# Kernel tuning notes

Measured on AMD Instinct MI355X. Metric: run time of the kernel, lower is better.

## Reference

```python
import jax, jax.numpy as jnp
import numpy as np

B, C, H, W = 8, 512, 64, 64
NUMS, V_C = 1024, 512
RATE = 0.999


def _normalize(x):
    # matches torch F.normalize(dim=-1, eps=1e-12)
    return x / jnp.clip(jnp.linalg.norm(x, axis=-1, keepdims=True), 1e-12)


def setup_inputs() -> dict:
    key = jax.random.key(0)
    k1, k2, k3 = jax.random.split(key, 3)
    return {
        "x": jax.random.normal(k1, (B, C, H, W), dtype=jnp.float32),
        "noise_feature": jax.random.normal(k2, (NUMS, C), dtype=jnp.float32),
        "std": jax.random.normal(k3, (NUMS, V_C), dtype=jnp.float32),
    }


def reference(x, noise_feature, std):
    b, c, h, w = x.shape
    # (b,c,h,w) -> (n,c)
    xf = jnp.transpose(x, (0, 2, 3, 1)).reshape(-1, c)
    m = jax.lax.stop_gradient(noise_feature)  # torch uses .data (no grad)
    xn = _normalize(xf)
    mn = _normalize(m)
    score = xn @ mn.T  # (n, k) cosine similarities

    # EMA codebook update (training path, update_flag=True)
    xd = jax.lax.stop_gradient(xf)
    embed_ind = jnp.argmax(score, axis=1)  # (n,)
    # segment_sum == x.T @ one_hot(ind), transposed; avoids dense one-hot GEMM
    embed_sum = jax.ops.segment_sum(xd, embed_ind, num_segments=NUMS)  # (k, c)
    counts = jax.ops.segment_sum(jnp.ones((xd.shape[0],), xd.dtype), embed_ind,
                                 num_segments=NUMS)  # (k,)
    embed_mean = embed_sum / (counts[:, None] + 1e-6)
    new_m = m * RATE + embed_mean * (1.0 - RATE)

    mn2 = _normalize(new_m)
    score2 = xn @ mn2.T  # (n, k)
    soft_label = jax.nn.softmax(score2, axis=1)
    out = (soft_label @ std).reshape(b, h, w, V_C)
    return out, score2
```

## Files before the change

### kernel.cpp

```cpp
#include <hip/hip_runtime.h>
#include <stdint.h>

#define NROWS 32768
#define CDIM  512
#define KCODES 1024
#define VC    512
#define LDP 72

typedef unsigned short u16;
typedef unsigned long long u64;
using bf16x8 = __attribute__((ext_vector_type(8))) __bf16;
using f32x4  = __attribute__((ext_vector_type(4))) float;

__device__ __forceinline__ float bf2f(u16 u){
  union { unsigned int i; float f; } x; x.i = ((unsigned int)u) << 16; return x.f;
}
__device__ __forceinline__ u16 f2bf(float f){
  union { float f; unsigned int i; } x; x.f = f;
  unsigned int u = x.i;
  u += 0x7fffu + ((u >> 16) & 1u);
  return (u16)(u >> 16);
}
__device__ __forceinline__ unsigned int pack2(u16 lo, u16 hi){
  return (unsigned int)lo | ((unsigned int)hi << 16);
}
__device__ __forceinline__ unsigned int fkey(float f){
  unsigned int u = __float_as_uint(f);
  return (u & 0x80000000u) ? ~u : (u | 0x80000000u);
}
__device__ __forceinline__ f32x4 mfma16(bf16x8 a, bf16x8 b, f32x4 c){
  return __builtin_amdgcn_mfma_f32_16x16x32_bf16(a, b, c, 0, 0, 0);
}
__device__ __forceinline__ void gload_lds16(const void* g, void* l){
  __builtin_amdgcn_global_load_lds(
      (const __attribute__((address_space(1))) unsigned int*)g,
      (__attribute__((address_space(3))) unsigned int*)l, 16, 0, 0);
}

__global__ __launch_bounds__(256) void k_transpose_x(const float* __restrict__ x,
                                                     u16* __restrict__ xf,
                                                     float* __restrict__ rsum){
  __shared__ float tile[64 * 64];
  int b  = blockIdx.z;
  int p0 = blockIdx.x * 64;
  int c0 = blockIdx.y * 64;
  int t  = threadIdx.x;
  const float* xb = x + (size_t)b * CDIM * 4096 + (size_t)c0 * 4096 + p0;

  int pl4 = (t & 15) * 4;
#pragma unroll
  for (int i = 0; i < 4; i++){
    int cl = i * 16 + (t >> 4);
    float4 v = *(const float4*)(xb + (size_t)cl * 4096 + pl4);
    *(float4*)(tile + cl * 64 + (pl4 ^ (cl & 0x38))) = v;
  }
  __syncthreads();

  int cl0 = (t & 7) * 8;
#pragma unroll
  for (int pass = 0; pass < 2; pass++){
    int pl = pass * 32 + (t >> 3);
    float v[8]; float s = 0.f;
#pragma unroll
    for (int j = 0; j < 8; j++){
      v[j] = tile[(cl0 + j) * 64 + (pl ^ cl0)];
      s += v[j] * v[j];
    }
    uint4 o;
    o.x = pack2(f2bf(v[0]), f2bf(v[1]));
    o.y = pack2(f2bf(v[2]), f2bf(v[3]));
    o.z = pack2(f2bf(v[4]), f2bf(v[5]));
    o.w = pack2(f2bf(v[6]), f2bf(v[7]));
    *(uint4*)(xf + (size_t)(b * 4096 + p0 + pl) * CDIM + c0 + cl0) = o;
    s += __shfl_xor(s, 1, 64);
    s += __shfl_xor(s, 2, 64);
    s += __shfl_xor(s, 4, 64);
    if ((t & 7) == 0) atomicAdd(rsum + b * 4096 + p0 + pl, s);
  }
}

__global__ __launch_bounds__(256) void k_rinv_fin(const float* __restrict__ rsum,
                                                  float* __restrict__ rinv){
  int i = blockIdx.x * 256 + threadIdx.x;
  rinv[i] = 1.0f / fmaxf(sqrtf(rsum[i]), 1e-12f);
}

__global__ __launch_bounds__(256) void k_norm_rows(const float* __restrict__ in,
                                                   u16* __restrict__ out){
  int row  = blockIdx.x * 4 + (threadIdx.x >> 6);
  int lane = threadIdx.x & 63;
  const float* r = in + (size_t)row * CDIM;
  float v[8]; float s = 0.f;
#pragma unroll
  for (int i = 0; i < 8; i++){ v[i] = r[lane + i * 64]; s += v[i] * v[i]; }
#pragma unroll
  for (int off = 32; off; off >>= 1) s += __shfl_xor(s, off, 64);
  float inv = 1.0f / fmaxf(sqrtf(s), 1e-12f);
#pragma unroll
  for (int i = 0; i < 8; i++) out[(size_t)row * CDIM + lane + i * 64] = f2bf(v[i] * inv);
}

__global__ __launch_bounds__(256) void k_transpose_std(const float* __restrict__ sd,
                                                       u16* __restrict__ stdT){
  __shared__ float tile[32][33];
  int k0 = blockIdx.x * 32;
  int v0 = blockIdx.y * 32;
  int tx = threadIdx.x, ty = threadIdx.y;
#pragma unroll
  for (int i = 0; i < 4; i++)
    tile[ty + i * 8][tx] = sd[(size_t)(k0 + ty + i * 8) * VC + v0 + tx];
  __syncthreads();
#pragma unroll
  for (int i = 0; i < 4; i++)
    stdT[(size_t)(v0 + ty + i * 8) * KCODES + k0 + tx] = f2bf(tile[tx][ty + i * 8]);
}

__global__ __launch_bounds__(256) void k_gemm1_am(const u16* __restrict__ xf,
                                                  const u16* __restrict__ mn,
                                                  u64* __restrict__ packed){
  __shared__ __align__(16) u16 As[128 * 64];
  __shared__ __align__(16) u16 Bs[128 * 64];
  int tid  = threadIdx.x;
  int wave = tid >> 6, lane = tid & 63;
  int wr = wave >> 1, wc = wave & 1;
  int quad = lane >> 4, l15 = lane & 15;
  int c0 = blockIdx.x * 128, r0 = blockIdx.y * 128;

  int srow = lane >> 3, schunk = lane & 7;
  const u16* ag = xf + (size_t)(r0 + wave * 8 + srow) * CDIM + schunk * 8;
  const u16* bg = mn + (size_t)(c0 + wave * 8 + srow) * CDIM + schunk * 8;
  u16* adst = As + wave * 8 * 64;
  u16* bdst = Bs + wave * 8 * 64;

  f32x4 acc[4][4];
#pragma unroll
  for (int rt = 0; rt < 4; rt++)
#pragma unroll
    for (int ct = 0; ct < 4; ct++) acc[rt][ct] = (f32x4)(0.f);

  for (int k0 = 0; k0 < CDIM; k0 += 64){
#pragma unroll
    for (int i = 0; i < 4; i++){
      gload_lds16(ag + (size_t)i * 32 * CDIM + k0, adst + i * 32 * 64);
      gload_lds16(bg + (size_t)i * 32 * CDIM + k0, bdst + i * 32 * 64);
    }
    __syncthreads();
#pragma unroll
    for (int ks = 0; ks < 2; ks++){
      bf16x8 af[4], bfr[4];
#pragma unroll
      for (int rt = 0; rt < 4; rt++)
        af[rt] = *(const bf16x8*)(As + (wr * 64 + rt * 16 + l15) * 64 + ks * 32 + quad * 8);
#pragma unroll
      for (int ct = 0; ct < 4; ct++)
        bfr[ct] = *(const bf16x8*)(Bs + (wc * 64 + ct * 16 + l15) * 64 + ks * 32 + quad * 8);
#pragma unroll
      for (int rt = 0; rt < 4; rt++)
#pragma unroll
        for (int ct = 0; ct < 4; ct++)
          acc[rt][ct] = mfma16(af[rt], bfr[ct], acc[rt][ct]);
    }
    __syncthreads();
  }

#pragma unroll
  for (int rt = 0; rt < 4; rt++){
#pragma unroll
    for (int q = 0; q < 4; q++){
      float bv = acc[rt][0][q];
      int   bc = c0 + wc * 64 + l15;
#pragma unroll
      for (int ct = 1; ct < 4; ct++){
        float v = acc[rt][ct][q];
        int   c = c0 + wc * 64 + ct * 16 + l15;
        if (v > bv){ bv = v; bc = c; }
      }
#pragma unroll
      for (int off = 1; off <= 8; off <<= 1){
        float ov = __shfl_xor(bv, off, 64);
        int   oc = __shfl_xor(bc, off, 64);
        if (ov > bv || (ov == bv && oc < bc)){ bv = ov; bc = oc; }
      }
      if (l15 == 0){
        int rg = r0 + wr * 64 + rt * 16 + quad * 4 + q;
        u64 key = ((u64)fkey(bv) << 32) | (unsigned int)(~(unsigned int)bc);
        atomicMax(packed + rg, key);
      }
    }
  }
}

__global__ __launch_bounds__(256) void k_gather(const u64* __restrict__ packed,
                                                const u16* __restrict__ xf,
                                                float* __restrict__ esum,
                                                float* __restrict__ counts){
  __shared__ float part[4][CDIM];
  __shared__ int   wcnt[4];
  int code = blockIdx.x;
  int tid = threadIdx.x, wave = tid >> 6, lane = tid & 63;
  float acc[8] = {0,0,0,0,0,0,0,0};
  int cnt = 0;
  for (int base = wave * 64; base < NROWS; base += 256){
    u64 pk = packed[base + lane];
    int cl = (int)(~(unsigned int)(pk & 0xffffffffull)) & (KCODES - 1);
    int match = (cl == code);
    u64 mask = __ballot(match);
    cnt += (int)__popcll(mask);
    while (mask){
      int b = __ffsll((long long)mask) - 1;
      mask &= mask - 1;
      int rr = base + b;
      uint4 v = *(const uint4*)(xf + (size_t)rr * CDIM + lane * 8);
      unsigned int w[4] = {v.x, v.y, v.z, v.w};
#pragma unroll
      for (int i = 0; i < 4; i++){
        acc[2 * i]     += bf2f((u16)(w[i] & 0xffffu));
        acc[2 * i + 1] += bf2f((u16)(w[i] >> 16));
      }
    }
  }
#pragma unroll
  for (int j = 0; j < 8; j++) part[wave][lane * 8 + j] = acc[j];
  if (lane == 0) wcnt[wave] = cnt;
  __syncthreads();
  for (int c = tid; c < CDIM; c += 256)
    esum[(size_t)code * CDIM + c] = part[0][c] + part[1][c] + part[2][c] + part[3][c];
  if (tid == 0) counts[code] = (float)(wcnt[0] + wcnt[1] + wcnt[2] + wcnt[3]);
}

__global__ __launch_bounds__(256) void k_newm(const float* __restrict__ m,
                                              const float* __restrict__ esum,
                                              const float* __restrict__ counts,
                                              u16* __restrict__ mn2){
  int row  = blockIdx.x * 4 + (threadIdx.x >> 6);
  int lane = threadIdx.x & 63;
  float cnt = counts[row];
  float sc  = 0.001f / (cnt + 1e-6f);
  float v[8]; float s = 0.f;
#pragma unroll
  for (int i = 0; i < 8; i++){
    int c = lane + i * 64;
    v[i] = m[(size_t)row * CDIM + c] * 0.999f + esum[(size_t)row * CDIM + c] * sc;
    s += v[i] * v[i];
  }
#pragma unroll
  for (int off = 32; off; off >>= 1) s += __shfl_xor(s, off, 64);
  float inv = 1.0f / fmaxf(sqrtf(s), 1e-12f);
#pragma unroll
  for (int i = 0; i < 8; i++) mn2[(size_t)row * CDIM + lane + i * 64] = f2bf(v[i] * inv);
}

__global__ __launch_bounds__(256) void k_gemm2(const u16* __restrict__ xf,
                                               const u16* __restrict__ mn2,
                                               const float* __restrict__ rinv,
                                               float* __restrict__ score2,
                                               float* __restrict__ pmax,
                                               float* __restrict__ psum){
  __shared__ __align__(16) u16 As[128 * 64];
  __shared__ __align__(16) u16 Bs[128 * 64];
  int tid  = threadIdx.x;
  int wave = tid >> 6, lane = tid & 63;
  int wr = wave >> 1, wc = wave & 1;
  int quad = lane >> 4, l15 = lane & 15;
  int c0 = blockIdx.x * 128, r0 = blockIdx.y * 128;

  int srow = lane >> 3, schunk = lane & 7;
  const u16* ag = xf  + (size_t)(r0 + wave * 8 + srow) * CDIM + schunk * 8;
  const u16* bg = mn2 + (size_t)(c0 + wave * 8 + srow) * CDIM + schunk * 8;
  u16* adst = As + wave * 8 * 64;
  u16* bdst = Bs + wave * 8 * 64;

  f32x4 acc[4][4];
#pragma unroll
  for (int rt = 0; rt < 4; rt++)
#pragma unroll
    for (int ct = 0; ct < 4; ct++) acc[rt][ct] = (f32x4)(0.f);

  for (int k0 = 0; k0 < CDIM; k0 += 64){
#pragma unroll
    for (int i = 0; i < 4; i++){
      gload_lds16(ag + (size_t)i * 32 * CDIM + k0, adst + i * 32 * 64);
      gload_lds16(bg + (size_t)i * 32 * CDIM + k0, bdst + i * 32 * 64);
    }
    __syncthreads();
#pragma unroll
    for (int ks = 0; ks < 2; ks++){
      bf16x8 af[4], bfr[4];
#pragma unroll
      for (int rt = 0; rt < 4; rt++)
        af[rt] = *(const bf16x8*)(As + (wr * 64 + rt * 16 + l15) * 64 + ks * 32 + quad * 8);
#pragma unroll
      for (int ct = 0; ct < 4; ct++)
        bfr[ct] = *(const bf16x8*)(Bs + (wc * 64 + ct * 16 + l15) * 64 + ks * 32 + quad * 8);
#pragma unroll
      for (int rt = 0; rt < 4; rt++)
#pragma unroll
        for (int ct = 0; ct < 4; ct++)
          acc[rt][ct] = mfma16(af[rt], bfr[ct], acc[rt][ct]);
    }
    __syncthreads();
  }

#pragma unroll
  for (int rt = 0; rt < 4; rt++){
#pragma unroll
    for (int q = 0; q < 4; q++){
      int grow = r0 + wr * 64 + rt * 16 + quad * 4 + q;
      float rv = rinv[grow];
      float v0 = acc[rt][0][q] * rv;
      float v1 = acc[rt][1][q] * rv;
      float v2 = acc[rt][2][q] * rv;
      float v3 = acc[rt][3][q] * rv;
      float* so = score2 + (size_t)grow * KCODES + c0 + wc * 64 + l15;
      so[0]  = v0;
      so[16] = v1;
      so[32] = v2;
      so[48] = v3;
      float mx = fmaxf(fmaxf(v0, v1), fmaxf(v2, v3));
#pragma unroll
      for (int off = 1; off <= 8; off <<= 1) mx = fmaxf(mx, __shfl_xor(mx, off, 64));
      float s = __expf(v0 - mx) + __expf(v1 - mx) + __expf(v2 - mx) + __expf(v3 - mx);
#pragma unroll
      for (int off = 1; off <= 8; off <<= 1) s += __shfl_xor(s, off, 64);
      if (l15 == 0){
        int pi = grow * 16 + blockIdx.x * 2 + wc;
        pmax[pi] = mx;
        psum[pi] = s;
      }
    }
  }
}

__global__ __launch_bounds__(256) void k_softcomb(const float* __restrict__ pmax,
                                                  const float* __restrict__ psum,
                                                  float* __restrict__ rowmax,
                                                  float* __restrict__ rsinv){
  int row = blockIdx.x * 256 + threadIdx.x;
  const float* pm = pmax + (size_t)row * 16;
  const float* ps = psum + (size_t)row * 16;
  float M = pm[0];
#pragma unroll
  for (int i = 1; i < 16; i++) M = fmaxf(M, pm[i]);
  float S = 0.f;
#pragma unroll
  for (int i = 0; i < 16; i++) S += ps[i] * __expf(pm[i] - M);
  rowmax[row] = M;
  rsinv[row]  = 1.0f / S;
}

__global__ __launch_bounds__(512) void k_gemm3(const float* __restrict__ score2,
                                               const float* __restrict__ rowmax,
                                               const float* __restrict__ rsinv,
                                               const u16* __restrict__ stdT,
                                               float* __restrict__ out){
  __shared__ __align__(16) u16 As[128 * LDP];
  __shared__ __align__(16) u16 Bs[256 * 64];
  int tid  = threadIdx.x;
  int wave = tid >> 6, lane = tid & 63;
  int wr = wave >> 2, wcol = wave & 3;
  int quad = lane >> 4, l15 = lane & 15;
  int c0 = blockIdx.x * 256, r0 = blockIdx.y * 128;
  int arow = tid >> 2, aq = tid & 3;

  int srow = lane >> 3, schunk = lane & 7;
  const u16* bg = stdT + (size_t)(c0 + wave * 8 + srow) * KCODES + schunk * 8;
  u16* bdst = Bs + wave * 8 * 64;

  float rmax = rowmax[r0 + arow];
  float rs   = rsinv [r0 + arow];

  f32x4 acc[4][4];
#pragma unroll
  for (int rt = 0; rt < 4; rt++)
#pragma unroll
    for (int ct = 0; ct < 4; ct++) acc[rt][ct] = (f32x4)(0.f);

  const float* ag = score2 + (size_t)(r0 + arow) * KCODES + aq * 16;

  for (int k0 = 0; k0 < KCODES; k0 += 64){
#pragma unroll
    for (int i = 0; i < 4; i++)
      gload_lds16(bg + (size_t)i * 64 * KCODES + k0, bdst + i * 64 * 64);
#pragma unroll
    for (int j = 0; j < 2; j++){
      float4 a = *(const float4*)(ag + k0 + j * 8);
      float4 b = *(const float4*)(ag + k0 + j * 8 + 4);
      uint4 o;
      o.x = pack2(f2bf(__expf(a.x - rmax) * rs), f2bf(__expf(a.y - rmax) * rs));
      o.y = pack2(f2bf(__expf(a.z - rmax) * rs), f2bf(__expf(a.w - rmax) * rs));
      o.z = pack2(f2bf(__expf(b.x - rmax) * rs), f2bf(__expf(b.y - rmax) * rs));
      o.w = pack2(f2bf(__expf(b.z - rmax) * rs), f2bf(__expf(b.w - rmax) * rs));
      *(uint4*)(As + arow * LDP + aq * 16 + j * 8) = o;
    }
    __syncthreads();
#pragma unroll
    for (int ks = 0; ks < 2; ks++){
      bf16x8 af[4], bfr[4];
#pragma unroll
      for (int rt = 0; rt < 4; rt++)
        af[rt] = *(const bf16x8*)(As + (wr * 64 + rt * 16 + l15) * LDP + ks * 32 + quad * 8);
#pragma unroll
      for (int ct = 0; ct < 4; ct++)
        bfr[ct] = *(const bf16x8*)(Bs + (wcol * 64 + ct * 16 + l15) * 64 + ks * 32 + quad * 8);
#pragma unroll
      for (int rt = 0; rt < 4; rt++)
#pragma unroll
        for (int ct = 0; ct < 4; ct++)
          acc[rt][ct] = mfma16(af[rt], bfr[ct], acc[rt][ct]);
    }
    __syncthreads();
  }
#pragma unroll
  for (int rt = 0; rt < 4; rt++){
#pragma unroll
    for (int q = 0; q < 4; q++){
      int grow = r0 + wr * 64 + rt * 16 + quad * 4 + q;
#pragma unroll
      for (int ct = 0; ct < 4; ct++){
        int gcol = c0 + wcol * 64 + ct * 16 + l15;
        out[(size_t)grow * VC + gcol] = acc[rt][ct][q];
      }
    }
  }
}

extern "C" void kernel_launch(void* const* d_in, const int* in_sizes, int n_in,
                              void* d_out, int out_size, void* d_ws, size_t ws_size,
                              hipStream_t stream){
  (void)in_sizes; (void)n_in; (void)out_size; (void)ws_size;
  const float* x      = (const float*)d_in[0];
  const float* m      = (const float*)d_in[1];
  const float* stdmat = (const float*)d_in[2];
  float* out    = (float*)d_out;
  float* score2 = out + (size_t)NROWS * VC;

  char* ws = (char*)d_ws;
  u16*   xf     = (u16*)  (ws + 0);
  u16*   mn     = (u16*)  (ws + 33554432);
  u16*   mn2    = (u16*)  (ws + 34603008);
  u16*   stdT   = (u16*)  (ws + 35651584);
  float* rinv   = (float*)(ws + 36700160);
  u64*   packed = (u64*)  (ws + 36831232);
  float* esum   = (float*)(ws + 37224448);
  float* counts = (float*)(ws + 39321600);
  float* rowmax = (float*)(ws + 39325696);
  float* rsinv  = (float*)(ws + 39456768);
  float* pmax   = (float*)(ws + 39587840);
  float* psum   = (float*)(ws + 41684992);
  float* rsum   = rowmax;

  hipMemsetAsync(packed, 0, (size_t)NROWS * 8, stream);
  hipMemsetAsync(rsum,   0, (size_t)NROWS * 4, stream);

  k_transpose_x  <<<dim3(64, 8, 8), 256, 0, stream>>>(x, xf, rsum);
  k_rinv_fin     <<<NROWS / 256, 256, 0, stream>>>(rsum, rinv);
  k_norm_rows    <<<KCODES / 4, 256, 0, stream>>>(m, mn);
  k_transpose_std<<<dim3(32, 16), dim3(32, 8), 0, stream>>>(stdmat, stdT);
  k_gemm1_am     <<<dim3(KCODES / 128, NROWS / 128), 256, 0, stream>>>(xf, mn, packed);
  k_gather       <<<KCODES, 256, 0, stream>>>(packed, xf, esum, counts);
  k_newm         <<<KCODES / 4, 256, 0, stream>>>(m, esum, counts, mn2);
  k_gemm2        <<<dim3(KCODES / 128, NROWS / 128), 256, 0, stream>>>(xf, mn2, rinv, score2, pmax, psum);
  k_softcomb     <<<NROWS / 256, 256, 0, stream>>>(pmax, psum, rowmax, rsinv);
  k_gemm3        <<<dim3(VC / 256, NROWS / 128), 512, 0, stream>>>(score2, rowmax, rsinv, stdT, out);
}
```

Measured before the change: 503.0 us.

## Widen softmax-GEMM tile to full output width and fuse small prep kernels

The final GEMM now gives each 512-thread block all 512 output columns. The fp32 score2 tile is read and exponentiated once per row instead of once per column half, which halves the traffic on the large score matrix and the softmax recomputation. The codebook-normalize and std-transpose kernels are merged into one launch. The row inverse-norm kernel is removed and its value is computed inline in the gemm2 epilogue from rsum. The trade-off is more accumulator registers and about 82KB of LDS per block, which lowers occupancy and leaves only one block per CU across a 256-block grid.

After: 514.1 us. 2.2% more time.

```diff
diff --git a/kernel.cpp b/kernel.cpp
--- a/kernel.cpp
+++ b/kernel.cpp
@@ -79,40 +79,37 @@
   }
 }
 
-__global__ __launch_bounds__(256) void k_rinv_fin(const float* __restrict__ rsum,
-                                                  float* __restrict__ rinv){
-  int i = blockIdx.x * 256 + threadIdx.x;
-  rinv[i] = 1.0f / fmaxf(sqrtf(rsum[i]), 1e-12f);
-}
-
-__global__ __launch_bounds__(256) void k_norm_rows(const float* __restrict__ in,
-                                                   u16* __restrict__ out){
-  int row  = blockIdx.x * 4 + (threadIdx.x >> 6);
-  int lane = threadIdx.x & 63;
-  const float* r = in + (size_t)row * CDIM;
-  float v[8]; float s = 0.f;
-#pragma unroll
-  for (int i = 0; i < 8; i++){ v[i] = r[lane + i * 64]; s += v[i] * v[i]; }
-#pragma unroll
-  for (int off = 32; off; off >>= 1) s += __shfl_xor(s, off, 64);
-  float inv = 1.0f / fmaxf(sqrtf(s), 1e-12f);
-#pragma unroll
-  for (int i = 0; i < 8; i++) out[(size_t)row * CDIM + lane + i * 64] = f2bf(v[i] * inv);
-}
-
-__global__ __launch_bounds__(256) void k_transpose_std(const float* __restrict__ sd,
-                                                       u16* __restrict__ stdT){
-  __shared__ float tile[32][33];
-  int k0 = blockIdx.x * 32;
-  int v0 = blockIdx.y * 32;
-  int tx = threadIdx.x, ty = threadIdx.y;
-#pragma unroll
-  for (int i = 0; i < 4; i++)
-    tile[ty + i * 8][tx] = sd[(size_t)(k0 + ty + i * 8) * VC + v0 + tx];
-  __syncthreads();
-#pragma unroll
-  for (int i = 0; i < 4; i++)
-    stdT[(size_t)(v0 + ty + i * 8) * KCODES + k0 + tx] = f2bf(tile[tx][ty + i * 8]);
+__global__ __launch_bounds__(256) void k_prep(const float* __restrict__ in,
+                                              u16* __restrict__ mn,
+                                              const float* __restrict__ sd,
+                                              u16* __restrict__ stdT){
+  int t = threadIdx.x;
+  if (blockIdx.x < 256){
+    int row  = blockIdx.x * 4 + (t >> 6);
+    int lane = t & 63;
+    const float* r = in + (size_t)row * CDIM;
+    float v[8]; float s = 0.f;
+#pragma unroll
+    for (int i = 0; i < 8; i++){ v[i] = r[lane + i * 64]; s += v[i] * v[i]; }
+#pragma unroll
+    for (int off = 32; off; off >>= 1) s += __shfl_xor(s, off, 64);
+    float inv = 1.0f / fmaxf(sqrtf(s), 1e-12f);
+#pragma unroll
+    for (int i = 0; i < 8; i++) mn[(size_t)row * CDIM + lane + i * 64] = f2bf(v[i] * inv);
+  } else {
+    __shared__ float tile[32][33];
+    int bid = blockIdx.x - 256;
+    int k0 = (bid & 31) * 32;
+    int v0 = (bid >> 5) * 32;
+    int tx = t & 31, ty = t >> 5;
+#pragma unroll
+    for (int i = 0; i < 4; i++)
+      tile[ty + i * 8][tx] = sd[(size_t)(k0 + ty + i * 8) * VC + v0 + tx];
+    __syncthreads();
+#pragma unroll
+    for (int i = 0; i < 4; i++)
+      stdT[(size_t)(v0 + ty + i * 8) * KCODES + k0 + tx] = f2bf(tile[tx][ty + i * 8]);
+  }
 }
 
 __global__ __launch_bounds__(256) void k_gemm1_am(const u16* __restrict__ xf,
@@ -252,7 +249,7 @@
 
 __global__ __launch_bounds__(256) void k_gemm2(const u16* __restrict__ xf,
                                                const u16* __restrict__ mn2,
-                                               const float* __restrict__ rinv,
+                                               const float* __restrict__ rsum,
                                                float* __restrict__ score2,
                                                float* __restrict__ pmax,
                                                float* __restrict__ psum){
@@ -306,7 +303,7 @@
 #pragma unroll
     for (int q = 0; q < 4; q++){
       int grow = r0 + wr * 64 + rt * 16 + quad * 4 + q;
-      float rv = rinv[grow];
+      float rv = 1.0f / fmaxf(sqrtf(rsum[grow]), 1e-12f);
       float v0 = acc[rt][0][q] * rv;
       float v1 = acc[rt][1][q] * rv;
       float v2 = acc[rt][2][q] * rv;
@@ -354,32 +351,32 @@
                                                const u16* __restrict__ stdT,
                                                float* __restrict__ out){
   __shared__ __align__(16) u16 As[128 * LDP];
-  __shared__ __align__(16) u16 Bs[256 * 64];
+  __shared__ __align__(16) u16 Bs[512 * 64];
   int tid  = threadIdx.x;
   int wave = tid >> 6, lane = tid & 63;
   int wr = wave >> 2, wcol = wave & 3;
   int quad = lane >> 4, l15 = lane & 15;
-  int c0 = blockIdx.x * 256, r0 = blockIdx.y * 128;
+  int r0 = blockIdx.x * 128;
   int arow = tid >> 2, aq = tid & 3;
 
   int srow = lane >> 3, schunk = lane & 7;
-  const u16* bg = stdT + (size_t)(c0 + wave * 8 + srow) * KCODES + schunk * 8;
+  const u16* bg = stdT + (size_t)(wave * 8 + srow) * KCODES + schunk * 8;
   u16* bdst = Bs + wave * 8 * 64;
 
   float rmax = rowmax[r0 + arow];
   float rs   = rsinv [r0 + arow];
 
-  f32x4 acc[4][4];
+  f32x4 acc[4][8];
 #pragma unroll
   for (int rt = 0; rt < 4; rt++)
 #pragma unroll
-    for (int ct = 0; ct < 4; ct++) acc[rt][ct] = (f32x4)(0.f);
+    for (int ct = 0; ct < 8; ct++) acc[rt][ct] = (f32x4)(0.f);
 
   const float* ag = score2 + (size_t)(r0 + arow) * KCODES + aq * 16;
 
   for (int k0 = 0; k0 < KCODES; k0 += 64){
 #pragma unroll
-    for (int i = 0; i < 4; i++)
+    for (int i = 0; i < 8; i++)
       gload_lds16(bg + (size_t)i * 64 * KCODES + k0, bdst + i * 64 * 64);
 #pragma unroll
     for (int j = 0; j < 2; j++){
@@ -395,18 +392,17 @@
     __syncthreads();
 #pragma unroll
     for (int ks = 0; ks < 2; ks++){
-      bf16x8 af[4], bfr[4];
+      bf16x8 af[4];
 #pragma unroll
       for (int rt = 0; rt < 4; rt++)
         af[rt] = *(const bf16x8*)(As + (wr * 64 + rt * 16 + l15) * LDP + ks * 32 + quad * 8);
 #pragma unroll
-      for (int ct = 0; ct < 4; ct++)
-        bfr[ct] = *(const bf16x8*)(Bs + (wcol * 64 + ct * 16 + l15) * 64 + ks * 32 + quad * 8);
-#pragma unroll
-      for (int rt = 0; rt < 4; rt++)
-#pragma unroll
-        for (int ct = 0; ct < 4; ct++)
-          acc[rt][ct] = mfma16(af[rt], bfr[ct], acc[rt][ct]);
+      for (int ct = 0; ct < 8; ct++){
+        bf16x8 bv = *(const bf16x8*)(Bs + (wcol * 128 + ct * 16 + l15) * 64 + ks * 32 + quad * 8);
+#pragma unroll
+        for (int rt = 0; rt < 4; rt++)
+          acc[rt][ct] = mfma16(af[rt], bv, acc[rt][ct]);
+      }
     }
     __syncthreads();
   }
@@ -416,8 +412,8 @@
     for (int q = 0; q < 4; q++){
       int grow = r0 + wr * 64 + rt * 16 + quad * 4 + q;
 #pragma unroll
-      for (int ct = 0; ct < 4; ct++){
-        int gcol = c0 + wcol * 64 + ct * 16 + l15;
+      for (int ct = 0; ct < 8; ct++){
+        int gcol = wcol * 128 + ct * 16 + l15;
         out[(size_t)grow * VC + gcol] = acc[rt][ct][q];
       }
     }
@@ -439,7 +435,6 @@
   u16*   mn     = (u16*)  (ws + 33554432);
   u16*   mn2    = (u16*)  (ws + 34603008);
   u16*   stdT   = (u16*)  (ws + 35651584);
-  float* rinv   = (float*)(ws + 36700160);
   u64*   packed = (u64*)  (ws + 36831232);
   float* esum   = (float*)(ws + 37224448);
   float* counts = (float*)(ws + 39321600);
@@ -453,13 +448,11 @@
   hipMemsetAsync(rsum,   0, (size_t)NROWS * 4, stream);
 
   k_transpose_x  <<<dim3(64, 8, 8), 256, 0, stream>>>(x, xf, rsum);
-  k_rinv_fin     <<<NROWS / 256, 256, 0, stream>>>(rsum, rinv);
-  k_norm_rows    <<<KCODES / 4, 256, 0, stream>>>(m, mn);
-  k_transpose_std<<<dim3(32, 16), dim3(32, 8), 0, stream>>>(stdmat, stdT);
+  k_prep         <<<768, 256, 0, stream>>>(m, mn, stdmat, stdT);
   k_gemm1_am     <<<dim3(KCODES / 128, NROWS / 128), 256, 0, stream>>>(xf, mn, packed);
   k_gather       <<<KCODES, 256, 0, stream>>>(packed, xf, esum, counts);
   k_newm         <<<KCODES / 4, 256, 0, stream>>>(m, esum, counts, mn2);
-  k_gemm2        <<<dim3(KCODES / 128, NROWS / 128), 256, 0, stream>>>(xf, mn2, rinv, score2, pmax, psum);
+  k_gemm2        <<<dim3(KCODES / 128, NROWS / 128), 256, 0, stream>>>(xf, mn2, rsum, score2, pmax, psum);
   k_softcomb     <<<NROWS / 256, 256, 0, stream>>>(pmax, psum, rowmax, rsinv);
-  k_gemm3        <<<dim3(VC / 256, NROWS / 128), 512, 0, stream>>>(score2, rowmax, rsinv, stdT, out);
-}
+  k_gemm3        <<<NROWS / 128, 512, 0, stream>>>(score2, rowmax, rsinv, stdT, out);
+}
```
